# Optimization experiments

Measured on AMD Instinct MI355X. Metric: run time of the kernel, lower is better.

The kernel has to match this reference:

```python
import jax, jax.numpy as jnp
import numpy as np

N_GROUP = 8
N_ITER = 3


def setup_inputs() -> dict:
    key = jax.random.key(0)
    x = jax.random.normal(key, (16, 64, 64, 512), dtype=jnp.float32)
    return {"x": x}


def reference(x):
    # x: [B, H, W, G*C] NHWC feature map
    B, H, W, Cg = x.shape
    G = N_GROUP
    C = Cg // G
    xr = x.reshape(B, H, W, G, C)  # [B,H,W,G,C]
    # routing logits per (batch, group); broadcastable against xr
    beta = jnp.zeros((B, 1, 1, G, 1), dtype=x.dtype)
    v = jnp.zeros((B, H, W, 1, C), dtype=x.dtype)
    for i in range(N_ITER):
        alpha = jax.nn.sigmoid(beta)                      # [B,1,1,G,1]
        v = jnp.sum(alpha * xr, axis=-2, keepdims=True)   # [B,H,W,1,C]
        if i < N_ITER - 1:
            # agreement: reduce over spatial dims and channels -> per (batch, group)
            beta = beta + jnp.sum(v * xr, axis=(1, 2, 4), keepdims=True)
    return v[..., 0, :]  # [B,H,W,C]
```

## Files before the change

kernel.cpp:

```cpp
#include <hip/hip_runtime.h>
#include <math.h>

#define BATCH        16
#define NPAIR        36
#define F4_PER_POS   128
#define F4_PER_GROUP 16
#define SLOTS_PER_B  65536
#define XB_F4        524288
#define BLOCKS_PER_B 64
#define NBLOCKS      (BATCH * BLOCKS_PER_B)

__global__ __launch_bounds__(256) void gram_kernel(const float* __restrict__ xf,
                                                   float* __restrict__ partials) {
    const float4* x = (const float4*)xf;
    const int b   = blockIdx.x >> 6;
    const int blk = blockIdx.x & 63;
    const float4* xb = x + (long)b * XB_F4;

    float acc[NPAIR];
#pragma unroll
    for (int p = 0; p < NPAIR; ++p) acc[p] = 0.f;

#pragma unroll
    for (int it = 0; it < 4; ++it) {
        const int t   = blk * 1024 + it * 256 + threadIdx.x;
        const int pos = t >> 4;
        const int c4  = t & 15;
        const float4* ptr = xb + pos * F4_PER_POS + c4;
        float4 xg[8];
#pragma unroll
        for (int g = 0; g < 8; ++g) xg[g] = ptr[g * F4_PER_GROUP];
        int p = 0;
#pragma unroll
        for (int g = 0; g < 8; ++g) {
#pragma unroll
            for (int gp = g; gp < 8; ++gp, ++p) {
                acc[p] += xg[g].x * xg[gp].x + xg[g].y * xg[gp].y +
                          xg[g].z * xg[gp].z + xg[g].w * xg[gp].w;
            }
        }
    }

#pragma unroll
    for (int p = 0; p < NPAIR; ++p) {
        float v = acc[p];
#pragma unroll
        for (int off = 32; off; off >>= 1) v += __shfl_xor(v, off, 64);
        acc[p] = v;
    }

    __shared__ float red[4][NPAIR];
    const int lane = threadIdx.x & 63;
    const int wave = threadIdx.x >> 6;
    if (lane == 0) {
#pragma unroll
        for (int p = 0; p < NPAIR; ++p) red[wave][p] = acc[p];
    }
    __syncthreads();
    if (threadIdx.x < NPAIR) {
        partials[blockIdx.x * NPAIR + threadIdx.x] =
            red[0][threadIdx.x] + red[1][threadIdx.x] +
            red[2][threadIdx.x] + red[3][threadIdx.x];
    }
}

__global__ __launch_bounds__(256) void out_kernel(const float* __restrict__ xf,
                                                  const float* __restrict__ partials,
                                                  float* __restrict__ outf) {
    const float4* x = (const float4*)xf;
    float4* out = (float4*)outf;
    const int b   = blockIdx.x >> 6;
    const int blk = blockIdx.x & 63;
    const float4* xb = x + (long)b * XB_F4;

    __shared__ float Sred[NPAIR];
    __shared__ float alpha1s[8];
    __shared__ float alpha2s[8];

    if (threadIdx.x < NPAIR) {
        float s = 0.f;
        const float* pb = partials + (long)b * BLOCKS_PER_B * NPAIR + threadIdx.x;
#pragma unroll 8
        for (int j = 0; j < BLOCKS_PER_B; ++j) s += pb[j * NPAIR];
        Sred[threadIdx.x] = s;
    }
    __syncthreads();

    const int g = threadIdx.x;
    float row[8];
    float beta1 = 0.f;
    if (g < 8) {
#pragma unroll
        for (int gp = 0; gp < 8; ++gp) {
            const int a  = g < gp ? g : gp;
            const int bb = g < gp ? gp : g;
            const int idx = a * 8 - (a * (a - 1)) / 2 + (bb - a);
            row[gp] = Sred[idx];
            beta1 += row[gp];
        }
        beta1 *= 0.5f;
        alpha1s[g] = 1.f / (1.f + expf(-beta1));
    }
    __syncthreads();
    if (g < 8) {
        float beta2 = beta1;
#pragma unroll
        for (int gp = 0; gp < 8; ++gp) beta2 += alpha1s[gp] * row[gp];
        alpha2s[g] = 1.f / (1.f + expf(-beta2));
    }
    __syncthreads();

    float a[8];
#pragma unroll
    for (int gg = 0; gg < 8; ++gg) a[gg] = alpha2s[gg];

#pragma unroll
    for (int it = 0; it < 4; ++it) {
        const int t   = blk * 1024 + it * 256 + threadIdx.x;
        const int pos = t >> 4;
        const int c4  = t & 15;
        const float4* ptr = xb + pos * F4_PER_POS + c4;
        float4 accv = make_float4(0.f, 0.f, 0.f, 0.f);
#pragma unroll
        for (int gg = 0; gg < 8; ++gg) {
            const float4 v = ptr[gg * F4_PER_GROUP];
            accv.x += a[gg] * v.x;
            accv.y += a[gg] * v.y;
            accv.z += a[gg] * v.z;
            accv.w += a[gg] * v.w;
        }
        out[(long)b * SLOTS_PER_B + t] = accv;
    }
}

extern "C" void kernel_launch(void* const* d_in, const int* in_sizes, int n_in,
                              void* d_out, int out_size, void* d_ws, size_t ws_size,
                              hipStream_t stream) {
    const float* x = (const float*)d_in[0];
    float* out = (float*)d_out;
    float* partials = (float*)d_ws;

    gram_kernel<<<NBLOCKS, 256, 0, stream>>>(x, partials);
    out_kernel<<<NBLOCKS, 256, 0, stream>>>(x, partials, out);
}
```

Before: 220.1 us.

## Compute routing weights once per batch in last gram block via ticket counter

```diff
diff --git a/kernel.cpp b/kernel.cpp
--- a/kernel.cpp
+++ b/kernel.cpp
@@ -10,8 +10,16 @@
 #define BLOCKS_PER_B 64
 #define NBLOCKS      (BATCH * BLOCKS_PER_B)
 
+typedef float nfloat4 __attribute__((ext_vector_type(4)));
+
+#define WS_PARTIALS  0
+#define WS_TICKETS   36864
+#define WS_ALPHA     36880
+
 __global__ __launch_bounds__(256) void gram_kernel(const float* __restrict__ xf,
-                                                   float* __restrict__ partials) {
+                                                   float* __restrict__ partials,
+                                                   unsigned int* __restrict__ tickets,
+                                                   float* __restrict__ alpha2) {
     const float4* x = (const float4*)xf;
     const int b   = blockIdx.x >> 6;
     const int blk = blockIdx.x & 63;
@@ -58,30 +66,35 @@
     }
     __syncthreads();
     if (threadIdx.x < NPAIR) {
-        partials[blockIdx.x * NPAIR + threadIdx.x] =
-            red[0][threadIdx.x] + red[1][threadIdx.x] +
-            red[2][threadIdx.x] + red[3][threadIdx.x];
+        const float v = red[0][threadIdx.x] + red[1][threadIdx.x] +
+                        red[2][threadIdx.x] + red[3][threadIdx.x];
+        __hip_atomic_store(&partials[blockIdx.x * NPAIR + threadIdx.x], v,
+                           __ATOMIC_RELAXED, __HIP_MEMORY_SCOPE_AGENT);
     }
-}
+    __syncthreads();
 
-__global__ __launch_bounds__(256) void out_kernel(const float* __restrict__ xf,
-                                                  const float* __restrict__ partials,
-                                                  float* __restrict__ outf) {
-    const float4* x = (const float4*)xf;
-    float4* out = (float4*)outf;
-    const int b   = blockIdx.x >> 6;
-    const int blk = blockIdx.x & 63;
-    const float4* xb = x + (long)b * XB_F4;
+    __shared__ int lastflag;
+    if (threadIdx.x == 0) {
+        __threadfence();
+        atomicCAS(&tickets[b], 0xAAAAAAAAu, 0u);
+        const unsigned int old =
+            __hip_atomic_fetch_add(&tickets[b], 1u, __ATOMIC_ACQ_REL,
+                                   __HIP_MEMORY_SCOPE_AGENT);
+        lastflag = (old == BLOCKS_PER_B - 1);
+    }
+    __syncthreads();
+    if (!lastflag) return;
 
+    __threadfence();
     __shared__ float Sred[NPAIR];
     __shared__ float alpha1s[8];
-    __shared__ float alpha2s[8];
-
     if (threadIdx.x < NPAIR) {
         float s = 0.f;
         const float* pb = partials + (long)b * BLOCKS_PER_B * NPAIR + threadIdx.x;
 #pragma unroll 8
-        for (int j = 0; j < BLOCKS_PER_B; ++j) s += pb[j * NPAIR];
+        for (int j = 0; j < BLOCKS_PER_B; ++j)
+            s += __hip_atomic_load(&pb[j * NPAIR], __ATOMIC_RELAXED,
+                                   __HIP_MEMORY_SCOPE_AGENT);
         Sred[threadIdx.x] = s;
     }
     __syncthreads();
@@ -106,13 +119,22 @@
         float beta2 = beta1;
 #pragma unroll
         for (int gp = 0; gp < 8; ++gp) beta2 += alpha1s[gp] * row[gp];
-        alpha2s[g] = 1.f / (1.f + expf(-beta2));
+        alpha2[b * 8 + g] = 1.f / (1.f + expf(-beta2));
     }
-    __syncthreads();
+}
+
+__global__ __launch_bounds__(256) void out_kernel(const float* __restrict__ xf,
+                                                  const float* __restrict__ alpha2,
+                                                  float* __restrict__ outf) {
+    const float4* x = (const float4*)xf;
+    nfloat4* out = (nfloat4*)outf;
+    const int b   = blockIdx.x >> 6;
+    const int blk = blockIdx.x & 63;
+    const float4* xb = x + (long)b * XB_F4;
 
     float a[8];
 #pragma unroll
-    for (int gg = 0; gg < 8; ++gg) a[gg] = alpha2s[gg];
+    for (int gg = 0; gg < 8; ++gg) a[gg] = alpha2[b * 8 + gg];
 
 #pragma unroll
     for (int it = 0; it < 4; ++it) {
@@ -129,7 +151,8 @@
             accv.z += a[gg] * v.z;
             accv.w += a[gg] * v.w;
         }
-        out[(long)b * SLOTS_PER_B + t] = accv;
+        nfloat4 nv = {accv.x, accv.y, accv.z, accv.w};
+        __builtin_nontemporal_store(nv, &out[(long)b * SLOTS_PER_B + t]);
     }
 }
 
@@ -138,8 +161,11 @@
                               hipStream_t stream) {
     const float* x = (const float*)d_in[0];
     float* out = (float*)d_out;
-    float* partials = (float*)d_ws;
+    float* ws = (float*)d_ws;
+    float* partials = ws + WS_PARTIALS;
+    unsigned int* tickets = (unsigned int*)(ws + WS_TICKETS);
+    float* alpha2 = ws + WS_ALPHA;
 
-    gram_kernel<<<NBLOCKS, 256, 0, stream>>>(x, partials);
-    out_kernel<<<NBLOCKS, 256, 0, stream>>>(x, partials, out);
+    gram_kernel<<<NBLOCKS, 256, 0, stream>>>(x, partials, tickets, alpha2);
+    out_kernel<<<NBLOCKS, 256, 0, stream>>>(x, alpha2, out);
 }
```

New measurement: 295.0 us. +34.0%, slower.
